# Optimization experiments

Hardware: AMD Instinct MI355X
Metric: run time of the kernel (lower is better)

Reference implementation:

```python
import jax, jax.numpy as jnp
import numpy as np

KH = KW = 3
STRIDE = 1
PAD = 1
DIL = 1
G = 4  # deformable groups


def setup_inputs() -> dict:
    key = jax.random.key(0)
    k1, k2, k3 = jax.random.split(key, 3)
    B, C, H, W = 8, 256, 64, 64
    K = KH * KW
    inp = jax.random.normal(k1, (B, C, H, W), dtype=jnp.float32)
    offset = jax.random.normal(k2, (B, 2 * G * K, H, W), dtype=jnp.float32)
    mask = jax.random.uniform(k3, (B, G * K, H, W), dtype=jnp.float32)
    return {"input": inp, "offset": offset, "mask": mask}


def _deform_sample(x, offset, mask):
    # x: [B,C,H,W]; offset: [B,2*G*K,Ho,Wo]; mask: [B,G*K,Ho,Wo]
    B, C, H, W = x.shape
    K = KH * KW
    Ho = (H + 2 * PAD - DIL * (KH - 1) - 1) // STRIDE + 1
    Wo = (W + 2 * PAD - DIL * (KW - 1) - 1) // STRIDE + 1
    Cg = C // G

    off = offset.reshape(B, G, K, 2, Ho, Wo)  # (dy, dx) per group/tap
    m = mask.reshape(B, G, K, Ho, Wo)

    # base sampling grid per kernel tap
    ky = (jnp.arange(KH) * DIL).repeat(KW)          # [K]
    kx = jnp.tile(jnp.arange(KW) * DIL, KH)          # [K]
    base_y = jnp.arange(Ho) * STRIDE - PAD           # [Ho]
    base_x = jnp.arange(Wo) * STRIDE - PAD           # [Wo]

    # sampling positions [B,G,K,Ho,Wo]
    py = base_y[None, None, None, :, None] + ky[None, None, :, None, None] + off[:, :, :, 0]
    px = base_x[None, None, None, None, :] + kx[None, None, :, None, None] + off[:, :, :, 1]

    y0 = jnp.floor(py).astype(jnp.int32)
    x0 = jnp.floor(px).astype(jnp.int32)
    ly = py - y0.astype(py.dtype)
    lx = px - x0.astype(px.dtype)

    xg = x.reshape(B, G, Cg, H * W)

    def gather(yy, xx, w):
        valid = (yy >= 0) & (yy < H) & (xx >= 0) & (xx < W)
        idx = jnp.clip(yy, 0, H - 1) * W + jnp.clip(xx, 0, W - 1)  # [B,G,K,Ho,Wo]
        g = jnp.take_along_axis(xg, idx.reshape(B, G, 1, -1), axis=3)
        g = g.reshape(B, G, Cg, K, Ho, Wo)
        return g * (w * valid.astype(w.dtype))[:, :, None]

    acc = gather(y0, x0, (1 - ly) * (1 - lx))
    acc = acc + gather(y0, x0 + 1, (1 - ly) * lx)
    acc = acc + gather(y0 + 1, x0, ly * (1 - lx))
    acc = acc + gather(y0 + 1, x0 + 1, ly * lx)

    # mask-weighted accumulation over kernel taps
    out = (acc * m[:, :, None]).sum(axis=3)  # [B,G,Cg,Ho,Wo]
    return out.reshape(B, C, Ho, Wo)


def reference(input, offset, mask):
    return _deform_sample(input, offset, mask)
```

## Files before the change

### kernel.cpp

```cpp
#include <hip/hip_runtime.h>
#include <hip/hip_fp16.h>

#define B_  8
#define C_  256
#define H_  64
#define W_  64
#define G_  4
#define CG_ 64
#define K_  9
#define HW_ (H_ * W_)

__global__ __launch_bounds__(256) void to_ghwc_f16(const float* __restrict__ in,
                                                   __half* __restrict__ out) {
  __shared__ unsigned int tile[32][65];
  const int b  = blockIdx.z;
  const int p0 = blockIdx.x * 64;
  const int g  = blockIdx.y;
  const int tid = threadIdx.x;
  const float* src = in + (size_t)b * C_ * HW_ + (size_t)g * CG_ * HW_;
  __half* dst = out + ((size_t)(b * G_ + g) * HW_) * CG_;

  const int px  = tid & 63;
  const int cp0 = tid >> 6;
#pragma unroll
  for (int i = 0; i < 8; ++i) {
    const int cp = cp0 + i * 4;
    const int c  = cp * 2;
    const float v0 = src[(size_t)c * HW_ + p0 + px];
    const float v1 = src[(size_t)(c + 1) * HW_ + p0 + px];
    const unsigned int lo = (unsigned int)__half_as_ushort(__float2half(v0));
    const unsigned int hi = (unsigned int)__half_as_ushort(__float2half(v1));
    tile[cp][px] = lo | (hi << 16);
  }
  __syncthreads();

  const int cpair = tid & 31;
  const int pr0   = tid >> 5;
#pragma unroll
  for (int i = 0; i < 8; ++i) {
    const int p = pr0 + i * 8;
    *(unsigned int*)(dst + (size_t)(p0 + p) * CG_ + 2 * cpair) = tile[cpair][p];
  }
}

union DeformSM {
  struct { int4 o[576]; float4 w[576]; } p;
  float ot[64][65];
};

__global__ __launch_bounds__(256, 4) void deform_g16(const __half* __restrict__ x,
                                                     const float* __restrict__ off,
                                                     const float* __restrict__ msk,
                                                     float* __restrict__ out) {
  __shared__ DeformSM sm;

  const int orig = blockIdx.x;
  const int wgid = (orig & 7) * 256 + (orig >> 3);
  const int tile = wgid & 63;
  const int bg   = wgid >> 6;
  const int ho0  = (tile >> 2) * 4;
  const int wo0  = (tile & 3) * 16;
  const int b    = bg >> 2;
  const int g    = bg & 3;
  const int tid  = threadIdx.x;

  for (int e = tid; e < 576; e += 256) {
    const int px  = e & 63;
    const int k   = e >> 6;
    const int row = px >> 4, col = px & 15;
    const int ho  = ho0 + row, wo = wo0 + col;
    const int ky = k / 3, kx = k - ky * 3;
    const int och = (g * K_ + k) * 2;
    const size_t ob = ((size_t)(b * (2 * G_ * K_) + och) * HW_) + ho * W_ + wo;
    const float dy = off[ob];
    const float dx = off[ob + HW_];
    const float m  = msk[((size_t)(b * (G_ * K_) + g * K_ + k) * HW_) + ho * W_ + wo];

    const float py  = (float)(ho - 1 + ky) + dy;
    const float pxx = (float)(wo - 1 + kx) + dx;
    const float fy = floorf(py), fx = floorf(pxx);
    const int y0 = (int)fy, x0 = (int)fx;
    const int y1 = y0 + 1,  x1 = x0 + 1;
    const float ly = py - fy, lx = pxx - fx;

    const bool vy0 = ((unsigned)y0 < (unsigned)H_), vy1 = ((unsigned)y1 < (unsigned)H_);
    const bool vx0 = ((unsigned)x0 < (unsigned)W_), vx1 = ((unsigned)x1 < (unsigned)W_);
    const float wy0 = (1.f - ly) * m, wy1 = ly * m;

    float4 w;
    w.x = (vy0 && vx0) ? wy0 * (1.f - lx) : 0.f;
    w.y = (vy0 && vx1) ? wy0 * lx         : 0.f;
    w.z = (vy1 && vx0) ? wy1 * (1.f - lx) : 0.f;
    w.w = (vy1 && vx1) ? wy1 * lx         : 0.f;

    const int y0c = min(max(y0, 0), H_ - 1), y1c = min(max(y1, 0), H_ - 1);
    const int x0c = min(max(x0, 0), W_ - 1), x1c = min(max(x1, 0), W_ - 1);

    int4 o;
    o.x = (y0c * W_ + x0c) << 7;
    o.y = (y0c * W_ + x1c) << 7;
    o.z = (y1c * W_ + x0c) << 7;
    o.w = (y1c * W_ + x1c) << 7;
    sm.p.o[e] = o;
    sm.p.w[e] = w;
  }
  __syncthreads();

  const int ci16 = (tid & 7) * 16;
  const int wi   = tid >> 3;
  const char* base = (const char*)x + (size_t)(b * G_ + g) * (HW_ * CG_ * 2);

  float a0[8] = {0.f, 0.f, 0.f, 0.f, 0.f, 0.f, 0.f, 0.f};
  float a1[8] = {0.f, 0.f, 0.f, 0.f, 0.f, 0.f, 0.f, 0.f};

#pragma unroll
  for (int k = 0; k < 9; ++k) {
    const int4   oA = sm.p.o[k * 64 + wi];
    const float4 wA = sm.p.w[k * 64 + wi];
    const int4   oB = sm.p.o[k * 64 + wi + 32];
    const float4 wB = sm.p.w[k * 64 + wi + 32];

    const float4 rA0 = *(const float4*)(base + (oA.x + ci16));
    const float4 rA1 = *(const float4*)(base + (oA.y + ci16));
    const float4 rA2 = *(const float4*)(base + (oA.z + ci16));
    const float4 rA3 = *(const float4*)(base + (oA.w + ci16));
    const float4 rB0 = *(const float4*)(base + (oB.x + ci16));
    const float4 rB1 = *(const float4*)(base + (oB.y + ci16));
    const float4 rB2 = *(const float4*)(base + (oB.z + ci16));
    const float4 rB3 = *(const float4*)(base + (oB.w + ci16));

    const __half* hA0 = (const __half*)&rA0;
    const __half* hA1 = (const __half*)&rA1;
    const __half* hA2 = (const __half*)&rA2;
    const __half* hA3 = (const __half*)&rA3;
    const __half* hB0 = (const __half*)&rB0;
    const __half* hB1 = (const __half*)&rB1;
    const __half* hB2 = (const __half*)&rB2;
    const __half* hB3 = (const __half*)&rB3;
#pragma unroll
    for (int j = 0; j < 8; ++j) {
      float s0 = a0[j];
      s0 = fmaf(wA.x, __half2float(hA0[j]), s0);
      s0 = fmaf(wA.y, __half2float(hA1[j]), s0);
      s0 = fmaf(wA.z, __half2float(hA2[j]), s0);
      s0 = fmaf(wA.w, __half2float(hA3[j]), s0);
      a0[j] = s0;
      float s1 = a1[j];
      s1 = fmaf(wB.x, __half2float(hB0[j]), s1);
      s1 = fmaf(wB.y, __half2float(hB1[j]), s1);
      s1 = fmaf(wB.z, __half2float(hB2[j]), s1);
      s1 = fmaf(wB.w, __half2float(hB3[j]), s1);
      a1[j] = s1;
    }
  }

  __syncthreads();
  {
    const int ci = tid & 7;
#pragma unroll
    for (int j = 0; j < 8; ++j) {
      sm.ot[ci * 8 + j][wi]      = a0[j];
      sm.ot[ci * 8 + j][wi + 32] = a1[j];
    }
  }
  __syncthreads();

  float* ob = out + ((size_t)(b * C_ + g * CG_)) * HW_;
#pragma unroll
  for (int q = 0; q < 16; ++q) {
    const int flat = q * 256 + tid;
    const int c  = flat >> 6;
    const int px = flat & 63;
    const int ho = ho0 + (px >> 4), wo = wo0 + (px & 15);
    ob[(size_t)c * HW_ + ho * W_ + wo] = sm.ot[c][px];
  }
}

__global__ __launch_bounds__(256) void deform_f32_nchw(const float* __restrict__ x,
                                                       const float* __restrict__ off,
                                                       const float* __restrict__ msk,
                                                       float* __restrict__ out) {
  __shared__ int4   s_o[144];
  __shared__ float4 s_w[144];
  const int woq = blockIdx.x;
  const int ho  = blockIdx.y;
  const int b   = blockIdx.z >> 2;
  const int g   = blockIdx.z & 3;
  const int tid = threadIdx.x;

  if (tid < 144) {
    const int wi = tid / 9, k = tid - wi * 9;
    const int wo = woq * 16 + wi;
    const int ky = k / 3, kx = k - ky * 3;
    const int och = (g * K_ + k) * 2;
    const size_t ob = ((size_t)(b * (2 * G_ * K_) + och) * H_ + ho) * W_ + wo;
    const float dy = off[ob];
    const float dx = off[ob + HW_];
    const float m  = msk[((size_t)(b * (G_ * K_) + g * K_ + k) * H_ + ho) * W_ + wo];
    const float py = (float)(ho - 1 + ky) + dy;
    const float px = (float)(wo - 1 + kx) + dx;
    const float fy = floorf(py), fx = floorf(px);
    const int y0 = (int)fy, x0 = (int)fx;
    const int y1 = y0 + 1,  x1 = x0 + 1;
    const float ly = py - fy, lx = px - fx;
    const bool vy0 = ((unsigned)y0 < (unsigned)H_), vy1 = ((unsigned)y1 < (unsigned)H_);
    const bool vx0 = ((unsigned)x0 < (unsigned)W_), vx1 = ((unsigned)x1 < (unsigned)W_);
    const float wy0 = (1.f - ly) * m, wy1 = ly * m;
    float4 w;
    w.x = (vy0 && vx0) ? wy0 * (1.f - lx) : 0.f;
    w.y = (vy0 && vx1) ? wy0 * lx         : 0.f;
    w.z = (vy1 && vx0) ? wy1 * (1.f - lx) : 0.f;
    w.w = (vy1 && vx1) ? wy1 * lx         : 0.f;
    const int y0c = min(max(y0, 0), H_ - 1), y1c = min(max(y1, 0), H_ - 1);
    const int x0c = min(max(x0, 0), W_ - 1), x1c = min(max(x1, 0), W_ - 1);
    s_o[tid] = make_int4(y0c * W_ + x0c, y0c * W_ + x1c, y1c * W_ + x0c, y1c * W_ + x1c);
    s_w[tid] = w;
  }
  __syncthreads();

  const int ci = tid & 15, wi = tid >> 4;
  const float* xb = x + (size_t)(b * C_ + g * CG_ + ci * 4) * HW_;
  float a0 = 0.f, a1 = 0.f, a2 = 0.f, a3 = 0.f;
#pragma unroll
  for (int k = 0; k < 9; ++k) {
    const int e = wi * 9 + k;
    const int4   o = s_o[e];
    const float4 w = s_w[e];
    a0 += w.x * xb[o.x] + w.y * xb[o.y] + w.z * xb[o.z] + w.w * xb[o.w];
    const float* x1p = xb + HW_;
    a1 += w.x * x1p[o.x] + w.y * x1p[o.y] + w.z * x1p[o.z] + w.w * x1p[o.w];
    const float* x2p = xb + 2 * HW_;
    a2 += w.x * x2p[o.x] + w.y * x2p[o.y] + w.z * x2p[o.z] + w.w * x2p[o.w];
    const float* x3p = xb + 3 * HW_;
    a3 += w.x * x3p[o.x] + w.y * x3p[o.y] + w.z * x3p[o.z] + w.w * x3p[o.w];
  }
  float* ob = out + ((size_t)(b * C_ + g * CG_ + ci * 4)) * HW_ + ho * W_ + woq * 16 + wi;
  ob[0] = a0; ob[HW_] = a1; ob[2 * HW_] = a2; ob[3 * HW_] = a3;
}

extern "C" void kernel_launch(void* const* d_in, const int* in_sizes, int n_in,
                              void* d_out, int out_size, void* d_ws, size_t ws_size,
                              hipStream_t stream) {
  const float* inp = (const float*)d_in[0];
  const float* off = (const float*)d_in[1];
  const float* msk = (const float*)d_in[2];
  float* out = (float*)d_out;

  const size_t need = (size_t)B_ * C_ * HW_ * sizeof(__half);
  if (ws_size >= need) {
    __half* xt = (__half*)d_ws;
    to_ghwc_f16<<<dim3(HW_ / 64, G_, B_), 256, 0, stream>>>(inp, xt);
    deform_g16<<<dim3(H_ * B_ * G_), 256, 0, stream>>>(xt, off, msk, out);
  } else {
    deform_f32_nchw<<<dim3(4, H_, B_ * G_), 256, 0, stream>>>(inp, off, msk, out);
  }
}
```

Baseline: 38.23 us.

## Shrink deform tiles to half-rows and write output directly without LDS transpose

Replaces the 4x16-pixel, 256-thread tile with a 32-pixel half-row tile of 128 threads, doubling the grid to 4096 blocks. The LDS output transpose and its two barriers are dropped; results are stored directly to NCHW, relying on 16 consecutive wo per channel being contiguous. The aim is more blocks for occupancy and less shared-memory traffic and synchronisation. The cost is less reuse of gathered neighbours between output rows and narrower, partly uncoalesced stores.

```diff
diff --git a/kernel.cpp b/kernel.cpp
--- a/kernel.cpp
+++ b/kernel.cpp
@@ -43,38 +43,32 @@
   }
 }
 
-union DeformSM {
-  struct { int4 o[576]; float4 w[576]; } p;
-  float ot[64][65];
-};
-
-__global__ __launch_bounds__(256, 4) void deform_g16(const __half* __restrict__ x,
+__global__ __launch_bounds__(128, 8) void deform_row(const __half* __restrict__ x,
                                                      const float* __restrict__ off,
                                                      const float* __restrict__ msk,
                                                      float* __restrict__ out) {
-  __shared__ DeformSM sm;
+  __shared__ int4   s_o[288];
+  __shared__ float4 s_w[288];
 
   const int orig = blockIdx.x;
-  const int wgid = (orig & 7) * 256 + (orig >> 3);
-  const int tile = wgid & 63;
-  const int bg   = wgid >> 6;
-  const int ho0  = (tile >> 2) * 4;
-  const int wo0  = (tile & 3) * 16;
+  const int wgid = (orig & 7) * 512 + (orig >> 3);
+  const int bg   = wgid >> 7;
+  const int loc  = wgid & 127;
+  const int ho   = loc >> 1;
+  const int wo0  = (loc & 1) * 32;
   const int b    = bg >> 2;
   const int g    = bg & 3;
   const int tid  = threadIdx.x;
 
-  for (int e = tid; e < 576; e += 256) {
-    const int px  = e & 63;
-    const int k   = e >> 6;
-    const int row = px >> 4, col = px & 15;
-    const int ho  = ho0 + row, wo = wo0 + col;
+  for (int e = tid; e < 288; e += 128) {
+    const int sl = e & 31;
+    const int k  = e >> 5;
+    const int wo = wo0 + sl;
     const int ky = k / 3, kx = k - ky * 3;
-    const int och = (g * K_ + k) * 2;
-    const size_t ob = ((size_t)(b * (2 * G_ * K_) + och) * HW_) + ho * W_ + wo;
+    const size_t ob = (size_t)(b * 72 + (g * 9 + k) * 2) * HW_ + ho * W_ + wo;
     const float dy = off[ob];
     const float dx = off[ob + HW_];
-    const float m  = msk[((size_t)(b * (G_ * K_) + g * K_ + k) * HW_) + ho * W_ + wo];
+    const float m  = msk[(size_t)(b * 36 + g * 9 + k) * HW_ + ho * W_ + wo];
 
     const float py  = (float)(ho - 1 + ky) + dy;
     const float pxx = (float)(wo - 1 + kx) + dx;
@@ -101,8 +95,8 @@
     o.y = (y0c * W_ + x1c) << 7;
     o.z = (y1c * W_ + x0c) << 7;
     o.w = (y1c * W_ + x1c) << 7;
-    sm.p.o[e] = o;
-    sm.p.w[e] = w;
+    s_o[e] = o;
+    s_w[e] = w;
   }
   __syncthreads();
 
@@ -115,10 +109,10 @@
 
 #pragma unroll
   for (int k = 0; k < 9; ++k) {
-    const int4   oA = sm.p.o[k * 64 + wi];
-    const float4 wA = sm.p.w[k * 64 + wi];
-    const int4   oB = sm.p.o[k * 64 + wi + 32];
-    const float4 wB = sm.p.w[k * 64 + wi + 32];
+    const int4   oA = s_o[k * 32 + wi];
+    const float4 wA = s_w[k * 32 + wi];
+    const int4   oB = s_o[k * 32 + wi + 16];
+    const float4 wB = s_w[k * 32 + wi + 16];
 
     const float4 rA0 = *(const float4*)(base + (oA.x + ci16));
     const float4 rA1 = *(const float4*)(base + (oA.y + ci16));
@@ -154,25 +148,12 @@
     }
   }
 
-  __syncthreads();
-  {
-    const int ci = tid & 7;
-#pragma unroll
-    for (int j = 0; j < 8; ++j) {
-      sm.ot[ci * 8 + j][wi]      = a0[j];
-      sm.ot[ci * 8 + j][wi + 32] = a1[j];
-    }
-  }
-  __syncthreads();
-
-  float* ob = out + ((size_t)(b * C_ + g * CG_)) * HW_;
-#pragma unroll
-  for (int q = 0; q < 16; ++q) {
-    const int flat = q * 256 + tid;
-    const int c  = flat >> 6;
-    const int px = flat & 63;
-    const int ho = ho0 + (px >> 4), wo = wo0 + (px & 15);
-    ob[(size_t)c * HW_ + ho * W_ + wo] = sm.ot[c][px];
+  float* ob = out + (size_t)(b * C_ + g * CG_) * HW_ + ho * W_ + wo0;
+#pragma unroll
+  for (int j = 0; j < 8; ++j) {
+    const int ch = (tid & 7) * 8 + j;
+    ob[(size_t)ch * HW_ + wi]      = a0[j];
+    ob[(size_t)ch * HW_ + wi + 16] = a1[j];
   }
 }
 
@@ -192,11 +173,10 @@
     const int wi = tid / 9, k = tid - wi * 9;
     const int wo = woq * 16 + wi;
     const int ky = k / 3, kx = k - ky * 3;
-    const int och = (g * K_ + k) * 2;
-    const size_t ob = ((size_t)(b * (2 * G_ * K_) + och) * H_ + ho) * W_ + wo;
+    const size_t ob = (size_t)(b * 72 + (g * 9 + k) * 2) * HW_ + ho * W_ + wo;
     const float dy = off[ob];
     const float dx = off[ob + HW_];
-    const float m  = msk[((size_t)(b * (G_ * K_) + g * K_ + k) * H_ + ho) * W_ + wo];
+    const float m  = msk[(size_t)(b * 36 + g * 9 + k) * HW_ + ho * W_ + wo];
     const float py = (float)(ho - 1 + ky) + dy;
     const float px = (float)(wo - 1 + kx) + dx;
     const float fy = floorf(py), fx = floorf(px);
@@ -234,7 +214,7 @@
     const float* x3p = xb + 3 * HW_;
     a3 += w.x * x3p[o.x] + w.y * x3p[o.y] + w.z * x3p[o.z] + w.w * x3p[o.w];
   }
-  float* ob = out + ((size_t)(b * C_ + g * CG_ + ci * 4)) * HW_ + ho * W_ + woq * 16 + wi;
+  float* ob = out + (size_t)(b * C_ + g * CG_ + ci * 4) * HW_ + ho * W_ + woq * 16 + wi;
   ob[0] = a0; ob[HW_] = a1; ob[2 * HW_] = a2; ob[3 * HW_] = a3;
 }
 
@@ -250,7 +230,7 @@
   if (ws_size >= need) {
     __half* xt = (__half*)d_ws;
     to_ghwc_f16<<<dim3(HW_ / 64, G_, B_), 256, 0, stream>>>(inp, xt);
-    deform_g16<<<dim3(H_ * B_ * G_), 256, 0, stream>>>(xt, off, msk, out);
+    deform_row<<<dim3(4096), 128, 0, stream>>>(xt, off, msk, out);
   } else {
     deform_f32_nchw<<<dim3(4, H_, B_ * G_), 256, 0, stream>>>(inp, off, msk, out);
   }
```

Result: slower. 47.42 us (+24.1%).
